# Optimization experiments

Hardware: AMD Instinct MI355X
Metric: run time of the kernel (lower is better)

The kernel has to match this reference:

```python
import jax, jax.numpy as jnp
import numpy as np

T, B, V, S = 800, 32, 1024, 100
BLANK = 0
LS = 0.1
NEG = -1e10  # finite 'log-zero' to keep grads NaN-free


def setup_inputs() -> dict:
    key = jax.random.key(0)
    k1, k2, k3, k4 = jax.random.split(key, 4)
    logits = jax.random.normal(k1, (T, B, V), jnp.float32)
    log_probs = jax.nn.log_softmax(logits, axis=-1)  # (T,B,V) as F.ctc_loss expects
    targets = jax.random.randint(k2, (B, S), 1, V)   # non-blank labels
    input_lengths = jax.random.randint(k3, (B,), T // 2, T + 1)
    target_lengths = jax.random.randint(k4, (B,), S // 2, S + 1)
    return dict(log_probs=log_probs, targets=targets,
                input_lengths=input_lengths, target_lengths=target_lengths)


def _ctc_loss_mean(log_probs, targets, input_lengths, target_lengths):
    # log_probs: (T,B,V); targets: (B,S)
    Tt, Bb, Vv = log_probs.shape
    Ss = targets.shape[1]
    L = 2 * Ss + 1  # extended label sequence: blank-interleaved
    ext = jnp.full((Bb, L), BLANK, dtype=targets.dtype).at[:, 1::2].set(targets)
    ext_prev2 = jnp.pad(ext[:, :-2], ((0, 0), (2, 0)), constant_values=BLANK)
    # transition s-2 -> s allowed only for non-blank labels differing from two back
    can_skip = (ext != BLANK) & (ext != ext_prev2)  # (B,L)

    def emit(lp_t):  # (B,V) -> (B,L) emission log-probs of extended labels
        return jnp.take_along_axis(lp_t, ext, axis=1)

    e0 = emit(log_probs[0])
    alpha0 = jnp.full((Bb, L), NEG, dtype=log_probs.dtype)
    alpha0 = alpha0.at[:, 0].set(e0[:, 0]).at[:, 1].set(e0[:, 1])

    def step(alpha, xs):
        lp_t, t = xs
        a1 = jnp.pad(alpha[:, :-1], ((0, 0), (1, 0)), constant_values=NEG)
        a2 = jnp.pad(alpha[:, :-2], ((0, 0), (2, 0)), constant_values=NEG)
        new = jnp.logaddexp(alpha, a1)
        new = jnp.where(can_skip, jnp.logaddexp(new, a2), new) + emit(lp_t)
        # freeze alpha for t >= input_length so final carry == alpha at len-1
        alpha = jnp.where((t < input_lengths)[:, None], new, alpha)
        return alpha, None

    alpha_T, _ = jax.lax.scan(step, alpha0, (log_probs[1:], jnp.arange(1, Tt)))

    idx = 2 * target_lengths  # final blank position in extended sequence
    a_blank = jnp.take_along_axis(alpha_T, idx[:, None], axis=1)[:, 0]
    a_label = jnp.take_along_axis(alpha_T, (idx - 1)[:, None], axis=1)[:, 0]
    nll = -jnp.logaddexp(a_blank, a_label)  # (B,)
    nll = jnp.where(nll > 1e9, 0.0, nll)    # zero_infinity
    # reduction='mean': per-sample loss / target_length, then batch mean
    return jnp.mean(nll / target_lengths.astype(log_probs.dtype))


def reference(log_probs, targets, input_lengths, target_lengths):
    ctc = _ctc_loss_mean(log_probs, targets, input_lengths, target_lengths)
    smooth = -jnp.mean(log_probs)
    return (1.0 - LS) * ctc + LS * smooth
```

## Files before the change

kernel.cpp:

```cpp
#include <hip/hip_runtime.h>
#include <hip/hip_bf16.h>

#define T_DIM 800
#define B_DIM 32
#define V_DIM 1024
#define S_DIM 100
#define L2E  1.4426950408889634f
#define LN2  0.6931471805599453f

#define NB1  1600
#define EOFF 4096
#define EROW 128
#define BROWS 801


__device__ __forceinline__ float dpp_shr1_f(float x) {
    return __int_as_float(__builtin_amdgcn_update_dpp(
        0, __float_as_int(x), 0x138, 0xF, 0xF, false));
}
__device__ __forceinline__ int dpp_shr1_i(int x) {
    return __builtin_amdgcn_update_dpp(0, x, 0x138, 0xF, 0xF, false);
}
__device__ __forceinline__ float rl50(float x) {
    return __int_as_float(__builtin_amdgcn_readlane(__float_as_int(x), 50));
}
__device__ __forceinline__ void gl16(const float* g, float* lds_dst) {
    __builtin_amdgcn_global_load_lds(
        (const __attribute__((address_space(1))) unsigned int*)g,
        (__attribute__((address_space(3))) unsigned int*)lds_dst,
        16, 0, 0);
}

extern "C" __global__ void __launch_bounds__(256)
ctc_prep(const float* __restrict__ lp,
         const int* __restrict__ tgt,
         float* __restrict__ ws)
{
    __shared__ float rowbuf[2][V_DIM];
    __shared__ float red[4];
    float* E = ws + EOFF;
    float* partials = ws + 1;
    const int bid = blockIdx.x;
    const int tid = threadIdx.x;
    const int b  = bid / 50;
    const int t0 = (bid - b * 50) * 16;
    const int* tg = tgt + b * S_DIM;

    float s = 0.0f;
    #pragma unroll 1
    for (int i = 0; i < 16; ++i) {
        const int t = t0 + i;
        const float4 v = ((const float4*)(lp + ((size_t)t * B_DIM + b) * V_DIM))[tid];
        s += (v.x + v.y) + (v.z + v.w);
        ((float4*)rowbuf[i & 1])[tid] = v;
        __syncthreads();
        if (tid < 64) {
            const float* rb = rowbuf[i & 1];
            const int m = tid;
            float a, c;
            if (m <= 49) {
                int2 t2 = ((const int2*)tg)[m];
                a = __builtin_amdgcn_exp2f(rb[t2.x] * L2E);
                c = __builtin_amdgcn_exp2f(rb[t2.y] * L2E);
            } else if (m == 50) {
                float ebv = __builtin_amdgcn_exp2f(rb[0] * L2E);
                a = ebv; c = ebv;
            } else {
                a = 0.0f; c = 0.0f;
            }
            ((float2*)(E + ((size_t)b * BROWS + t) * EROW))[m] = make_float2(a, c);
        }
    }
    for (int off = 32; off; off >>= 1) s += __shfl_down(s, off, 64);
    if ((tid & 63) == 0) red[tid >> 6] = s;
    __syncthreads();
    if (tid == 0) partials[bid] = (red[0] + red[1]) + (red[2] + red[3]);
}

extern "C" __global__ void __launch_bounds__(64)
ctc_rec(const int* __restrict__ tgt,
        const int* __restrict__ ilen,
        const int* __restrict__ tlen,
        float* __restrict__ ws,
        float* __restrict__ out)
{
    __shared__ float bufA[32 * EROW];
    __shared__ float bufB[32 * EROW];
    unsigned int* cnt = (unsigned int*)ws;
    float* partials = ws + 1;
    float* nlls = ws + 1 + NB1;
    const int b = blockIdx.x;
    const int l = threadIdx.x;
    const float* E = ws + EOFF + (size_t)b * BROWS * EROW;
    const int* tg = tgt + b * S_DIM;
    const int len = ilen[b];
    const int tl  = tlen[b];
    const int steps = len - 1;

    float cs1f = 0, cs3f = 0;
    if (l <= 49) {
        int v1 = tg[2 * l];
        int vp = (l >= 1) ? tg[2 * l - 1] : -1;
        cs1f = (v1 != vp) ? 1.0f : 0.0f;
        int v3 = tg[2 * l + 1];
        cs3f = (v3 != v1) ? 1.0f : 0.0f;
    }

    float p0 = 0, p1 = 0, p2 = 0, p3 = 0;
    float qv = 0, sff = 0, sfg = 0;
    int   el = 0, eLp = 0;
    {
        float2 q0 = ((const float2*)E)[l];
        float eb0 = rl50(q0.x);
        p0 = (l == 0) ? eb0  : 0.0f;
        p1 = (l == 0) ? q0.x : 0.0f;
    }

    float2 ga0, ga1, ga2, ga3, gb0, gb1, gb2, gb3;

#define STAGE(BUF, SB) do { \
    const int tb_ = 1 + 32 * (SB); \
    _Pragma("unroll") \
    for (int g_ = 0; g_ < 16; ++g_) { \
        gl16(E + (size_t)(tb_ + 2 * g_) * EROW + 4 * l, &BUF[g_ * 256]); \
    } \
} while (0)

#define WAIT0 do { \
    asm volatile("s_waitcnt vmcnt(0)" ::: "memory"); \
    __builtin_amdgcn_sched_barrier(0); \
} while (0)

#define PREF_(BUF, G, R0, R1, R2, R3) do { \
    const float2* bp_ = (const float2*)(BUF); \
    R0 = bp_[(4 * (G) + 0) * 64 + l]; \
    R1 = bp_[(4 * (G) + 1) * 64 + l]; \
    R2 = bp_[(4 * (G) + 2) * 64 + l]; \
    R3 = bp_[(4 * (G) + 3) * 64 + l]; \
} while (0)

#define BD do { \
    float mz_ = fmaxf(fmaxf(p0, p1), fmaxf(p2, p3)); \
    int dead_ = (mz_ == 0.0f) ? 1 : 0; \
    int er_ = (int)((__float_as_uint(mz_) >> 23) & 255u); \
    unsigned fld_ = dead_ ? 127u : (unsigned)(254 - er_); \
    float sc_ = __uint_as_float(fld_ << 23); \
    p0 *= sc_; p1 *= sc_; p2 *= sc_; p3 *= sc_; \
    el += dead_ ? 0 : (er_ - 127); \
    int e1s_ = dpp_shr1_i(el); \
    int elA_ = dead_ ? e1s_ : el; \
    int e2s_ = dpp_shr1_i(elA_); \
    int elB_ = dead_ ? e2s_ : el; \
    int e3s_ = dpp_shr1_i(elB_); \
    int d1_ = e3s_ - elB_; d1_ = d1_ < -120 ? -120 : (d1_ > 120 ? 120 : d1_); \
    int d2_ = eLp  - elB_; d2_ = d2_ < -120 ? -120 : (d2_ > 120 ? 120 : d2_); \
    sfg = (l == 0) ? 0.0f : __uint_as_float((unsigned)(d1_ + 127) << 23); \
    sff = (l == 0) ? 0.0f : __uint_as_float((unsigned)(d2_ + 127) << 23); \
    el = elB_; eLp = e3s_; \
} while (0)

#define ST(SF, Q, EBS) do { \
    float h3_ = qv * (SF); \
    float vown_ = fmaf(cs3f, p1, p2 + p3); \
    float n3_ = vown_ * (Q).y; \
    float n0_ = (p0 + h3_) * (EBS); \
    float n1_ = fmaf(cs1f, h3_, p0 + p1) * (Q).x; \
    float n2_ = (p1 + p2) * (EBS); \
    qv = dpp_shr1_f(n3_); \
    p0 = n0_; p1 = n1_; p2 = n2_; p3 = n3_; \
} while (0)

#define GRP_(R0, R1, R2, R3) do { \
    BD; \
    ST(sff, R0, rl50(R0.x)); \
    ST(sfg, R1, rl50(R1.x)); \
    ST(sfg, R2, rl50(R2.x)); \
    ST(sfg, R3, rl50(R3.x)); \
} while (0)

#define GRPT_(R0, R1, R2, R3, BASE) do { \
    if ((BASE) < nst) { \
        BD; \
        ST(sff, R0, rl50(R0.x)); \
        if ((BASE) + 1 < nst) ST(sfg, R1, rl50(R1.x)); \
        if ((BASE) + 2 < nst) ST(sfg, R2, rl50(R2.x)); \
        if ((BASE) + 3 < nst) ST(sfg, R3, rl50(R3.x)); \
    } \
} while (0)

#define CONS_FULL(BUF) do { \
    PREF_(BUF, 0, ga0, ga1, ga2, ga3); \
    PREF_(BUF, 1, gb0, gb1, gb2, gb3); GRP_(ga0, ga1, ga2, ga3); \
    PREF_(BUF, 2, ga0, ga1, ga2, ga3); GRP_(gb0, gb1, gb2, gb3); \
    PREF_(BUF, 3, gb0, gb1, gb2, gb3); GRP_(ga0, ga1, ga2, ga3); \
    PREF_(BUF, 4, ga0, ga1, ga2, ga3); GRP_(gb0, gb1, gb2, gb3); \
    PREF_(BUF, 5, gb0, gb1, gb2, gb3); GRP_(ga0, ga1, ga2, ga3); \
    PREF_(BUF, 6, ga0, ga1, ga2, ga3); GRP_(gb0, gb1, gb2, gb3); \
    PREF_(BUF, 7, gb0, gb1, gb2, gb3); GRP_(ga0, ga1, ga2, ga3); \
    GRP_(gb0, gb1, gb2, gb3); \
} while (0)

#define CONS_TAIL(BUF) do { \
    PREF_(BUF, 0, ga0, ga1, ga2, ga3); \
    PREF_(BUF, 1, gb0, gb1, gb2, gb3); GRPT_(ga0, ga1, ga2, ga3, 0); \
    PREF_(BUF, 2, ga0, ga1, ga2, ga3); GRPT_(gb0, gb1, gb2, gb3, 4); \
    PREF_(BUF, 3, gb0, gb1, gb2, gb3); GRPT_(ga0, ga1, ga2, ga3, 8); \
    PREF_(BUF, 4, ga0, ga1, ga2, ga3); GRPT_(gb0, gb1, gb2, gb3, 12); \
    PREF_(BUF, 5, gb0, gb1, gb2, gb3); GRPT_(ga0, ga1, ga2, ga3, 16); \
    PREF_(BUF, 6, ga0, ga1, ga2, ga3); GRPT_(gb0, gb1, gb2, gb3, 20); \
    PREF_(BUF, 7, gb0, gb1, gb2, gb3); GRPT_(ga0, ga1, ga2, ga3, 24); \
    GRPT_(gb0, gb1, gb2, gb3, 28); \
} while (0)

    const int nfull = steps >> 5;
    const int nst   = steps & 31;

    STAGE(bufA, 0);
    WAIT0;
    int sb = 0;
    #pragma unroll 1
    for (; sb + 2 <= nfull; sb += 2) {
        STAGE(bufB, sb + 1);
        CONS_FULL(bufA);
        WAIT0;
        STAGE(bufA, sb + 2);
        CONS_FULL(bufB);
        WAIT0;
    }
    if (sb < nfull) {
        STAGE(bufB, sb + 1);
        CONS_FULL(bufA);
        WAIT0;
        CONS_TAIL(bufB);
    } else {
        CONS_TAIL(bufA);
    }

    int idx = 2 * tl;
    int lanehi = idx >> 2, rhi = idx & 3;
    int lanelo = (idx - 1) >> 2, rlo = (idx - 1) & 3;
    float q0 = __shfl(p0, lanehi, 64), q1 = __shfl(p1, lanehi, 64);
    float q2 = __shfl(p2, lanehi, 64), q3 = __shfl(p3, lanehi, 64);
    int   eh = __shfl(el, lanehi, 64);
    float ph = (rhi == 0) ? q0 : (rhi == 1) ? q1 : (rhi == 2) ? q2 : q3;
    float g0 = __shfl(p0, lanelo, 64), g1 = __shfl(p1, lanelo, 64);
    float g2 = __shfl(p2, lanelo, 64), g3 = __shfl(p3, lanelo, 64);
    int   eo = __shfl(el, lanelo, 64);
    float pl = (rlo == 0) ? g0 : (rlo == 1) ? g1 : (rlo == 2) ? g2 : g3;
    float vhi = (ph > 0.0f) ? __builtin_amdgcn_logf(ph) + (float)eh : -3.0e9f;
    float vlo = (pl > 0.0f) ? __builtin_amdgcn_logf(pl) + (float)eo : -3.0e9f;
    float m = fmaxf(vhi, vlo);
    float d = fminf(vhi, vlo) - m;
    float ll2 = m + __builtin_amdgcn_logf(1.0f + __builtin_amdgcn_exp2f(d));
    float nll = -ll2 * LN2;
    if (!(nll < 1e9f)) nll = 0.0f;

    int last = 0;
    if (l == 0) {
        nlls[b] = nll;
        __threadfence();
        unsigned old = __hip_atomic_fetch_add(cnt, 1u, __ATOMIC_ACQ_REL,
                                              __HIP_MEMORY_SCOPE_AGENT);
        last = (old == B_DIM - 1) ? 1 : 0;
    }
    last = __shfl(last, 0, 64);
    if (last) {
        float ps = 0.0f;
        for (int i = l; i < NB1; i += 64) ps += partials[i];
        for (int off = 32; off; off >>= 1) ps += __shfl_down(ps, off, 64);
        float cs = 0.0f;
        if (l < B_DIM) cs = nlls[l] / (float)tlen[l];
        for (int off = 32; off; off >>= 1) cs += __shfl_down(cs, off, 64);
        if (l == 0) {
            float smooth = -ps / (float)((long long)T_DIM * B_DIM * V_DIM);
            float ctc = cs / (float)B_DIM;
            out[0] = 0.9f * ctc + 0.1f * smooth;
        }
    }
}

extern "C" void kernel_launch(void* const* d_in, const int* in_sizes, int n_in,
                              void* d_out, int out_size, void* d_ws, size_t ws_size,
                              hipStream_t stream) {
    const float* lp  = (const float*)d_in[0];
    const int* tgt   = (const int*)d_in[1];
    const int* ilen  = (const int*)d_in[2];
    const int* tlen  = (const int*)d_in[3];
    float* out = (float*)d_out;
    float* ws  = (float*)d_ws;
    hipMemsetAsync(d_ws, 0, 4, stream);
    ctc_prep<<<NB1, 256, 0, stream>>>(lp, tgt, ws);
    ctc_rec<<<B_DIM, 64, 0, stream>>>(tgt, ilen, tlen, ws, out);
}
```

Baseline: 75.97 us.

## Split prep rows across waves, drop block barriers, zero counter in kernel

The prep kernel now gives each of its four wavefronts four time rows. Each wave loads full rows into a private LDS buffer and computes the emission gathers itself, so the per-row __syncthreads and the single-wave bottleneck on the exp gathers go away. Target indices are loaded once per thread instead of once per row. The separate memset launch is replaced by block 0 zeroing the counter inside the prep kernel. This relies on stream ordering before ctc_rec reads the counter, and LDS use grows to 32KB per block, which may limit occupancy.

```diff
diff --git a/kernel.cpp b/kernel.cpp
--- a/kernel.cpp
+++ b/kernel.cpp
@@ -36,43 +36,43 @@
          const int* __restrict__ tgt,
          float* __restrict__ ws)
 {
-    __shared__ float rowbuf[2][V_DIM];
+    __shared__ float rb[4][2][V_DIM];
     __shared__ float red[4];
     float* E = ws + EOFF;
     float* partials = ws + 1;
     const int bid = blockIdx.x;
     const int tid = threadIdx.x;
+    const int w = tid >> 6, j = tid & 63;
     const int b  = bid / 50;
-    const int t0 = (bid - b * 50) * 16;
+    const int t0 = (bid - b * 50) * 16 + w * 4;
     const int* tg = tgt + b * S_DIM;
 
+    if (bid == 0 && tid == 0) ((unsigned int*)ws)[0] = 0;
+
+    int c1 = 0, c2 = 0;
+    if (j <= 49) { int2 t2 = ((const int2*)tg)[j]; c1 = t2.x; c2 = t2.y; }
+
     float s = 0.0f;
-    #pragma unroll 1
-    for (int i = 0; i < 16; ++i) {
+    #pragma unroll
+    for (int i = 0; i < 4; ++i) {
         const int t = t0 + i;
-        const float4 v = ((const float4*)(lp + ((size_t)t * B_DIM + b) * V_DIM))[tid];
-        s += (v.x + v.y) + (v.z + v.w);
-        ((float4*)rowbuf[i & 1])[tid] = v;
-        __syncthreads();
-        if (tid < 64) {
-            const float* rb = rowbuf[i & 1];
-            const int m = tid;
-            float a, c;
-            if (m <= 49) {
-                int2 t2 = ((const int2*)tg)[m];
-                a = __builtin_amdgcn_exp2f(rb[t2.x] * L2E);
-                c = __builtin_amdgcn_exp2f(rb[t2.y] * L2E);
-            } else if (m == 50) {
-                float ebv = __builtin_amdgcn_exp2f(rb[0] * L2E);
-                a = ebv; c = ebv;
-            } else {
-                a = 0.0f; c = 0.0f;
-            }
-            ((float2*)(E + ((size_t)b * BROWS + t) * EROW))[m] = make_float2(a, c);
-        }
+        const float4* src = (const float4*)(lp + ((size_t)t * B_DIM + b) * V_DIM);
+        float4 va = src[j], vb = src[j + 64], vc = src[j + 128], vd = src[j + 192];
+        s += ((va.x + va.y) + (va.z + va.w)) + ((vb.x + vb.y) + (vb.z + vb.w))
+           + ((vc.x + vc.y) + (vc.z + vc.w)) + ((vd.x + vd.y) + (vd.z + vd.w));
+        float* rw = rb[w][i & 1];
+        ((float4*)rw)[j] = va; ((float4*)rw)[j + 64] = vb;
+        ((float4*)rw)[j + 128] = vc; ((float4*)rw)[j + 192] = vd;
+        float a, c;
+        if (j <= 49)      { a = __builtin_amdgcn_exp2f(rw[c1] * L2E);
+                            c = __builtin_amdgcn_exp2f(rw[c2] * L2E); }
+        else if (j == 50) { float ebv = __builtin_amdgcn_exp2f(rw[0] * L2E);
+                            a = ebv; c = ebv; }
+        else              { a = 0.0f; c = 0.0f; }
+        ((float2*)(E + ((size_t)b * BROWS + t) * EROW))[j] = make_float2(a, c);
     }
     for (int off = 32; off; off >>= 1) s += __shfl_down(s, off, 64);
-    if ((tid & 63) == 0) red[tid >> 6] = s;
+    if (j == 0) red[w] = s;
     __syncthreads();
     if (tid == 0) partials[bid] = (red[0] + red[1]) + (red[2] + red[3]);
 }
@@ -288,7 +288,6 @@
     const int* tlen  = (const int*)d_in[3];
     float* out = (float*)d_out;
     float* ws  = (float*)d_ws;
-    hipMemsetAsync(d_ws, 0, 4, stream);
     ctc_prep<<<NB1, 256, 0, stream>>>(lp, tgt, ws);
     ctc_rec<<<B_DIM, 64, 0, stream>>>(tgt, ilen, tlen, ws, out);
 }
```

Measured after the change: 72.20 us. 1.05x faster.
